# Performance work log

Hardware: AMD Instinct MI355X
Metric: run time of the kernel (lower is better)

## Reference

```python
import jax, jax.numpy as jnp
import numpy as np

D = 768
H = 12
DH = D // H  # 64
LN_EPS = 1e-5


def layer_norm(x, gamma, beta):
    mu = jnp.mean(x, axis=-1, keepdims=True)
    var = jnp.var(x, axis=-1, keepdims=True)
    return (x - mu) * jax.lax.rsqrt(var + LN_EPS) * gamma + beta


def setup_inputs() -> dict:
    key = jax.random.key(0)
    ks = jax.random.split(key, 12)
    b, n1, n2 = 2, 4096, 4096
    s = 1.0 / np.sqrt(D)
    return {
        "input_cap": jax.random.normal(ks[0], (b, n1, D), jnp.float32),
        "output_cap": jax.random.normal(ks[1], (b, n2, D), jnp.float32),
        "Wq": jax.random.normal(ks[2], (D, D), jnp.float32) * s,
        "bq": jnp.zeros((D,), jnp.float32),
        "Wk": jax.random.normal(ks[3], (D, D), jnp.float32) * s,
        "bk": jnp.zeros((D,), jnp.float32),
        "Wv": jax.random.normal(ks[4], (D, D), jnp.float32) * s,
        "bv": jnp.zeros((D,), jnp.float32),
        "ln_g": jnp.ones((D,), jnp.float32),
        "ln_b": jnp.zeros((D,), jnp.float32),
        "Wp": jax.random.normal(ks[5], (D, D), jnp.float32) * s,
        "bp": jnp.zeros((D,), jnp.float32),
    }


def reference(input_cap, output_cap, Wq, bq, Wk, bk, Wv, bv, ln_g, ln_b, Wp, bp):
    b, n1, _ = input_cap.shape
    n2 = output_cap.shape[1]
    i = layer_norm(input_cap, ln_g, ln_b)   # shared LayerNorm, as in source
    o = layer_norm(output_cap, ln_g, ln_b)
    q = (o @ Wq.T + bq).reshape(b, n2, H, DH).transpose(0, 2, 1, 3)  # b h n2 dh
    k = (i @ Wk.T + bk).reshape(b, n1, H, DH).transpose(0, 2, 1, 3)  # b h n1 dh
    v = (i @ Wv.T + bv).reshape(b, n1, H, DH).transpose(0, 2, 1, 3)  # b h n1 dh
    scores = jnp.einsum("bhqd,bhkd->bhqk", q, k) / np.sqrt(DH)
    probs = jax.nn.softmax(scores, axis=-1)
    ctl = jnp.einsum("bhqk,bhkd->bhqd", probs, v)
    ctl = ctl.transpose(0, 2, 1, 3).reshape(b, n2, D)
    # DropPath is identity in eval mode
    return output_cap + ctl @ Wp.T + bp
```

## Files before the change

kernel.cpp:

```cpp
#include <hip/hip_runtime.h>


#define D 768
#define LDP 72
#define L2E 1.4426950408889634f
#define NW 589824

typedef unsigned int u32;
typedef unsigned short u16;
typedef short bf16x8 __attribute__((ext_vector_type(8)));
typedef float f32x4 __attribute__((ext_vector_type(4)));
typedef float f32x16 __attribute__((ext_vector_type(16)));
typedef u16 u16x4 __attribute__((ext_vector_type(4)));
typedef u32 u32x4 __attribute__((ext_vector_type(4)));
typedef float f32x4v __attribute__((ext_vector_type(4)));

static __device__ __forceinline__ u16 f2bf(float f) {
  u32 b = __builtin_bit_cast(u32, f);
  b += 0x7FFFu + ((b >> 16) & 1u);
  return (u16)(b >> 16);
}

static __device__ __forceinline__ u32 cvtpk(float lo, float hi) {
  u32 r;
  asm("v_cvt_pk_bf16_f32 %0, %1, %2" : "=v"(r) : "v"(lo), "v"(hi));
  return r;
}

static __device__ __forceinline__ void plswap(u32& a, u32& b) {
  asm("v_permlane32_swap_b32 %0, %1" : "+v"(a), "+v"(b));
}

#define MFMA16(a, b, c) __builtin_amdgcn_mfma_f32_16x16x32_bf16((a), (b), (c), 0, 0, 0)
#define MFMA32(a, b, c) __builtin_amdgcn_mfma_f32_32x32x16_bf16((a), (b), (c), 0, 0, 0)

__global__ __launch_bounds__(256) void ln_kernel(
    const float* __restrict__ icap, const float* __restrict__ ocap,
    const float* __restrict__ g, const float* __restrict__ be,
    u16* __restrict__ iln, u16* __restrict__ oln) {
  int r = blockIdx.x;
  const float* src; u16* dst; int rr;
  if (r < 8192) { src = icap; dst = iln; rr = r; }
  else          { src = ocap; dst = oln; rr = r - 8192; }
  const float* row = src + (size_t)rr * D;
  int t = threadIdx.x;
  float x0 = row[t], x1 = row[t + 256], x2 = row[t + 512];
  float s = x0 + x1 + x2;
  float q = x0 * x0 + x1 * x1 + x2 * x2;
#pragma unroll
  for (int off = 32; off > 0; off >>= 1) {
    s += __shfl_xor(s, off);
    q += __shfl_xor(q, off);
  }
  __shared__ float red[8];
  int w = t >> 6, lane = t & 63;
  if (lane == 0) { red[w] = s; red[4 + w] = q; }
  __syncthreads();
  s = red[0] + red[1] + red[2] + red[3];
  q = red[4] + red[5] + red[6] + red[7];
  float mu = s * (1.0f / 768.0f);
  float var = q * (1.0f / 768.0f) - mu * mu;
  float rs = rsqrtf(var + 1e-5f);
  u16* drow = dst + (size_t)rr * D;
  drow[t]       = f2bf((x0 - mu) * rs * g[t]       + be[t]);
  drow[t + 256] = f2bf((x1 - mu) * rs * g[t + 256] + be[t + 256]);
  drow[t + 512] = f2bf((x2 - mu) * rs * g[t + 512] + be[t + 512]);
}

__global__ __launch_bounds__(256) void wcast_kernel(
    const float* __restrict__ w0, const float* __restrict__ w1,
    const float* __restrict__ w2, const float* __restrict__ w3,
    u16* __restrict__ dst) {
  int wsel = blockIdx.y;
  const float* src = wsel == 0 ? w0 : wsel == 1 ? w1 : wsel == 2 ? w2 : w3;
  int i = (blockIdx.x * 256 + threadIdx.x) * 4;
  f32x4v v = *(const f32x4v*)(src + i);
  u16x4 o = { f2bf(v[0]), f2bf(v[1]), f2bf(v[2]), f2bf(v[3]) };
  *(u16x4*)(dst + (size_t)wsel * NW + i) = o;
}

static __device__ __forceinline__ void gemm_core_128(
    const u16* __restrict__ A, const u16* __restrict__ W,
    int mrow0, int nrow0, f32x4 (&acc)[4][4]) {
  __shared__ __align__(16) u16 As[128][LDP];
  __shared__ __align__(16) u16 Bs[128][LDP];
  const int tid = threadIdx.x;
  const int lane = tid & 63;
  const int w = tid >> 6;
  const int wr = (w >> 1) << 6, wc = (w & 1) << 6;
  const int l15 = lane & 15, lg = lane >> 4;

  for (int kt = 0; kt < D; kt += 64) {
#pragma unroll
    for (int it = 0; it < 4; ++it) {
      int idx = it * 256 + tid;
      int row = idx >> 3, c8 = (idx & 7) << 3;
      uint4 va = *(const uint4*)(A + (size_t)(mrow0 + row) * D + kt + c8);
      uint4 vb = *(const uint4*)(W + (size_t)(nrow0 + row) * D + kt + c8);
      *(uint4*)&As[row][c8] = va;
      *(uint4*)&Bs[row][c8] = vb;
    }
    __syncthreads();
    bf16x8 af[4][2];
#pragma unroll
    for (int m = 0; m < 4; ++m) {
#pragma unroll
      for (int c = 0; c < 2; ++c)
        af[m][c] = *(const bf16x8*)&As[wr + m * 16 + l15][c * 32 + lg * 8];
    }
#pragma unroll
    for (int n = 0; n < 4; ++n) {
      bf16x8 b0 = *(const bf16x8*)&Bs[wc + n * 16 + l15][lg * 8];
      bf16x8 b1 = *(const bf16x8*)&Bs[wc + n * 16 + l15][32 + lg * 8];
#pragma unroll
      for (int m = 0; m < 4; ++m) {
        acc[m][n] = MFMA16(af[m][0], b0, acc[m][n]);
        acc[m][n] = MFMA16(af[m][1], b1, acc[m][n]);
      }
    }
    __syncthreads();
  }
}

__global__ __launch_bounds__(256) void qkv_gemm(
    const u16* __restrict__ i_ln, const u16* __restrict__ o_ln,
    const u16* __restrict__ Wb,
    const float* __restrict__ bq, const float* __restrict__ bk,
    const float* __restrict__ bv,
    u16* __restrict__ qout, u16* __restrict__ kout, u16* __restrict__ vT) {
  const int mblk = blockIdx.x;
  const int ny = blockIdx.y;
  const int which = ny / 6;
  const int nb = ny % 6;
  const u16* A = (which == 0) ? o_ln : i_ln;
  const u16* W = Wb + (size_t)which * NW;
  const float* bias = (which == 0) ? bq : (which == 1) ? bk : bv;

  const f32x4 z = {0.f, 0.f, 0.f, 0.f};
  f32x4 acc[4][4];
#pragma unroll
  for (int m = 0; m < 4; ++m)
#pragma unroll
    for (int n = 0; n < 4; ++n) acc[m][n] = z;

  gemm_core_128(A, W, mblk * 128, nb * 128, acc);

  const int lane = threadIdx.x & 63, w = threadIdx.x >> 6;
  const int wr = (w >> 1) << 6, wc = (w & 1) << 6;
  const int l15 = lane & 15, lg = lane >> 4;
  const int m0 = mblk * 128 + wr;
  const int n0 = nb * 128 + wc;

  if (which == 2) {
#pragma unroll
    for (int m = 0; m < 4; ++m) {
#pragma unroll
      for (int n = 0; n < 4; ++n) {
        int gn = n0 + n * 16 + l15;
        float bi = bias[gn];
        int gm = m0 + m * 16 + lg * 4;
        int bidx = gm >> 12, seq = gm & 4095;
        u16x4 pk = { f2bf(acc[m][n][0] + bi), f2bf(acc[m][n][1] + bi),
                     f2bf(acc[m][n][2] + bi), f2bf(acc[m][n][3] + bi) };
        *(u16x4*)(vT + ((size_t)bidx * 768 + gn) * 4096 + seq) = pk;
      }
    }
  } else {
    u16* out = (which == 0) ? qout : kout;
    const float scale = (which == 0) ? 0.125f : 1.0f;
#pragma unroll
    for (int m = 0; m < 4; ++m) {
#pragma unroll
      for (int n = 0; n < 4; ++n) {
        int gn = n0 + n * 16 + l15;
        float bi = bias[gn];
#pragma unroll
        for (int r = 0; r < 4; ++r) {
          int gm = m0 + m * 16 + lg * 4 + r;
          out[(size_t)gm * D + gn] = f2bf((acc[m][n][r] + bi) * scale);
        }
      }
    }
  }
}

__global__ __launch_bounds__(256) void proj_gemm(
    const u16* __restrict__ ctl, const u16* __restrict__ Wpb,
    const float* __restrict__ bp, const float* __restrict__ res,
    float* __restrict__ out) {
  const int mblk = blockIdx.x;
  const int nb = blockIdx.y;
  const f32x4 z = {0.f, 0.f, 0.f, 0.f};
  f32x4 acc[4][4];
#pragma unroll
  for (int m = 0; m < 4; ++m)
#pragma unroll
    for (int n = 0; n < 4; ++n) acc[m][n] = z;

  gemm_core_128(ctl, Wpb, mblk * 128, nb * 128, acc);

  const int lane = threadIdx.x & 63, w = threadIdx.x >> 6;
  const int wr = (w >> 1) << 6, wc = (w & 1) << 6;
  const int l15 = lane & 15, lg = lane >> 4;
  const int m0 = mblk * 128 + wr;
  const int n0 = nb * 128 + wc;
#pragma unroll
  for (int m = 0; m < 4; ++m) {
#pragma unroll
    for (int n = 0; n < 4; ++n) {
      int gn = n0 + n * 16 + l15;
      float bi = bp[gn];
#pragma unroll
      for (int r = 0; r < 4; ++r) {
        int gm = m0 + m * 16 + lg * 4 + r;
        out[(size_t)gm * D + gn] = res[(size_t)gm * D + gn] + acc[m][n][r] + bi;
      }
    }
  }
}

__global__ __launch_bounds__(256, 3) void attn_kernel(
    const u16* __restrict__ q, const u16* __restrict__ k,
    const u16* __restrict__ vT, u16* __restrict__ ctl) {
  const int qb = blockIdx.x;
  const int bh = blockIdx.y;
  const int b = bh / 12, h = bh % 12;
  const int tid = threadIdx.x;
  const int lane = tid & 63, w = tid >> 6;
  const int l31 = lane & 31;
  const int hi = lane >> 5;
  const int swz = l31 & 7;

  __shared__ __align__(16) u16 Ks[64 * 64];
  __shared__ __align__(16) u16 Vs[64 * 64];

  const int qrow0 = qb * 128 + w * 32;
  const u16* qbase = q + (size_t)b * 4096 * D + h * 64;
  const u16* kbase = k + (size_t)b * 4096 * D + h * 64;
  const u16* vbase = vT + ((size_t)b * 768 + h * 64) * 4096;

  bf16x8 qf[4];
#pragma unroll
  for (int ks = 0; ks < 4; ++ks)
    qf[ks] = *(const bf16x8*)(qbase + (size_t)(qrow0 + l31) * D + ks * 16 + hi * 8);

  f32x16 acc[2];
#pragma unroll
  for (int db = 0; db < 2; ++db)
#pragma unroll
    for (int r = 0; r < 16; ++r) acc[db][r] = 0.f;
  float m = -1e30f, l = 0.f;

  for (int kv0 = 0; kv0 < 4096; kv0 += 64) {
#pragma unroll
    for (int it = 0; it < 2; ++it) {
      int idx = it * 256 + tid;
      int row = idx >> 3, c16 = idx & 7;
      int sc = c16 ^ (row & 7);
      uint4 vk = *(const uint4*)(kbase + (size_t)(kv0 + row) * D + c16 * 8);
      uint4 vv = *(const uint4*)(vbase + (size_t)row * 4096 + kv0 + c16 * 8);
      *(uint4*)&Ks[row * 64 + sc * 8] = vk;
      *(uint4*)&Vs[row * 64 + sc * 8] = vv;
    }
    __syncthreads();

    f32x16 st[2];
#pragma unroll
    for (int t = 0; t < 2; ++t) {
      f32x16 s;
#pragma unroll
      for (int r = 0; r < 16; ++r) s[r] = 0.f;
#pragma unroll
      for (int ks = 0; ks < 4; ++ks) {
        bf16x8 kf = *(const bf16x8*)&Ks[(t * 32 + l31) * 64 + ((2 * ks + hi) ^ swz) * 8];
        s = MFMA32(kf, qf[ks], s);
      }
      st[t] = s;
    }

    float pm = st[0][0];
#pragma unroll
    for (int t = 0; t < 2; ++t)
#pragma unroll
      for (int r = 0; r < 16; ++r) pm = fmaxf(pm, st[t][r]);
    { u32 a = __builtin_bit_cast(u32, pm), bb = a;
      plswap(a, bb);
      float po = __builtin_bit_cast(float, hi ? a : bb);
      pm = fmaxf(pm, po); }

    if (pm > m + 8.0f) {
      float es = __builtin_amdgcn_exp2f((m - pm) * L2E);
      m = pm;
      l *= es;
#pragma unroll
      for (int db = 0; db < 2; ++db)
#pragma unroll
        for (int r = 0; r < 16; ++r) acc[db][r] *= es;
    }
    float mL2 = m * L2E;

    float ls = 0.f;
    bf16x8 pf[4];
#pragma unroll
    for (int t = 0; t < 2; ++t) {
      float p[16];
#pragma unroll
      for (int r = 0; r < 16; ++r) {
        p[r] = __builtin_amdgcn_exp2f(st[t][r] * L2E - mL2);
        ls += p[r];
      }
      u32 a0 = cvtpk(p[0], p[1]),   a1 = cvtpk(p[2], p[3]);
      u32 b0 = cvtpk(p[4], p[5]),   b1 = cvtpk(p[6], p[7]);
      plswap(a0, b0); plswap(a1, b1);
      u32x4 w0 = {a0, a1, b0, b1};
      pf[2 * t] = __builtin_bit_cast(bf16x8, w0);
      u32 c0 = cvtpk(p[8], p[9]),   c1 = cvtpk(p[10], p[11]);
      u32 d0 = cvtpk(p[12], p[13]), d1 = cvtpk(p[14], p[15]);
      plswap(c0, d0); plswap(c1, d1);
      u32x4 w1 = {c0, c1, d0, d1};
      pf[2 * t + 1] = __builtin_bit_cast(bf16x8, w1);
    }
    { u32 a = __builtin_bit_cast(u32, ls), bb = a;
      plswap(a, bb);
      float lo = __builtin_bit_cast(float, hi ? a : bb);
      ls += lo; }
    l += ls;

#pragma unroll
    for (int db = 0; db < 2; ++db)
#pragma unroll
      for (int ks = 0; ks < 4; ++ks) {
        bf16x8 vf = *(const bf16x8*)&Vs[(db * 32 + l31) * 64 + ((2 * ks + hi) ^ swz) * 8];
        acc[db] = MFMA32(vf, pf[ks], acc[db]);
      }
    __syncthreads();
  }

  float inv = 1.0f / l;
  u16* cbase = ctl + ((size_t)b * 4096 + qrow0 + l31) * D + h * 64;
#pragma unroll
  for (int db = 0; db < 2; ++db)
#pragma unroll
    for (int rq = 0; rq < 4; ++rq) {
      u16x4 pkv = { f2bf(acc[db][rq * 4 + 0] * inv), f2bf(acc[db][rq * 4 + 1] * inv),
                    f2bf(acc[db][rq * 4 + 2] * inv), f2bf(acc[db][rq * 4 + 3] * inv) };
      *(u16x4*)(cbase + db * 32 + rq * 8 + hi * 4) = pkv;
    }
}

extern "C" void kernel_launch(void* const* d_in, const int* in_sizes, int n_in,
                              void* d_out, int out_size, void* d_ws, size_t ws_size,
                              hipStream_t stream) {
  const float* in_cap  = (const float*)d_in[0];
  const float* out_cap = (const float*)d_in[1];
  const float* Wq = (const float*)d_in[2];
  const float* bq = (const float*)d_in[3];
  const float* Wk = (const float*)d_in[4];
  const float* bk = (const float*)d_in[5];
  const float* Wv = (const float*)d_in[6];
  const float* bv = (const float*)d_in[7];
  const float* ln_g = (const float*)d_in[8];
  const float* ln_b = (const float*)d_in[9];
  const float* Wp = (const float*)d_in[10];
  const float* bp = (const float*)d_in[11];
  float* out = (float*)d_out;

  char* ws = (char*)d_ws;
  const size_t tsz = (size_t)8192 * D * 2;
  u16* i_ln = (u16*)(ws + 0 * tsz);
  u16* o_ln = (u16*)(ws + 1 * tsz);
  u16* qb_  = (u16*)(ws + 2 * tsz);
  u16* kb_  = (u16*)(ws + 3 * tsz);
  u16* vT   = (u16*)(ws + 4 * tsz);
  u16* ctl  = (u16*)(ws + 5 * tsz);
  u16* Wb   = (u16*)(ws + 6 * tsz);

  ln_kernel<<<dim3(16384), dim3(256), 0, stream>>>(in_cap, out_cap, ln_g, ln_b, i_ln, o_ln);
  wcast_kernel<<<dim3(576, 4), dim3(256), 0, stream>>>(Wq, Wk, Wv, Wp, Wb);
  qkv_gemm<<<dim3(64, 18), dim3(256), 0, stream>>>(i_ln, o_ln, Wb, bq, bk, bv, qb_, kb_, vT);
  attn_kernel<<<dim3(32, 24), dim3(256), 0, stream>>>(qb_, kb_, vT, ctl);
  proj_gemm<<<dim3(64, 6), dim3(256), 0, stream>>>(ctl, Wb + (size_t)3 * NW, bp, out_cap, out);
}
```

Baseline: 344.0 us.

## Use direct global-to-LDS loads in GEMM and prefetch K/V tiles in attention

In the projection GEMM core, the register-staged tile copy is replaced with global_load_lds 16-byte direct loads into unpadded 64-wide LDS tiles. The attention loop now prefetches the next K/V tile into registers while the current tile is computed, which overlaps global load latency with MFMA work. The loop also wraps the MFMA sections in s_setprio and splits the max and sum reductions into four independent chains to shorten dependency chains. Dropping the LDS row padding may add bank conflicts on fragment reads, and the prefetch raises register pressure.

```diff
diff --git a/kernel.cpp b/kernel.cpp
--- a/kernel.cpp
+++ b/kernel.cpp
@@ -2,7 +2,6 @@
 
 
 #define D 768
-#define LDP 72
 #define L2E 1.4426950408889634f
 #define NW 589824
 
@@ -29,6 +28,12 @@
 
 static __device__ __forceinline__ void plswap(u32& a, u32& b) {
   asm("v_permlane32_swap_b32 %0, %1" : "+v"(a), "+v"(b));
+}
+
+static __device__ __forceinline__ void gload_lds16(const u16* g, u16* l) {
+  __builtin_amdgcn_global_load_lds(
+      (const __attribute__((address_space(1))) unsigned int*)g,
+      (__attribute__((address_space(3))) unsigned int*)l, 16, 0, 0);
 }
 
 #define MFMA16(a, b, c) __builtin_amdgcn_mfma_f32_16x16x32_bf16((a), (b), (c), 0, 0, 0)
@@ -82,23 +87,23 @@
 static __device__ __forceinline__ void gemm_core_128(
     const u16* __restrict__ A, const u16* __restrict__ W,
     int mrow0, int nrow0, f32x4 (&acc)[4][4]) {
-  __shared__ __align__(16) u16 As[128][LDP];
-  __shared__ __align__(16) u16 Bs[128][LDP];
+  __shared__ __align__(1024) u16 As[128 * 64];
+  __shared__ __align__(1024) u16 Bs[128 * 64];
   const int tid = threadIdx.x;
   const int lane = tid & 63;
   const int w = tid >> 6;
   const int wr = (w >> 1) << 6, wc = (w & 1) << 6;
   const int l15 = lane & 15, lg = lane >> 4;
+  const int lr = lane >> 3, lc = (lane & 7) << 3;
 
   for (int kt = 0; kt < D; kt += 64) {
 #pragma unroll
-    for (int it = 0; it < 4; ++it) {
-      int idx = it * 256 + tid;
-      int row = idx >> 3, c8 = (idx & 7) << 3;
-      uint4 va = *(const uint4*)(A + (size_t)(mrow0 + row) * D + kt + c8);
-      uint4 vb = *(const uint4*)(W + (size_t)(nrow0 + row) * D + kt + c8);
-      *(uint4*)&As[row][c8] = va;
-      *(uint4*)&Bs[row][c8] = vb;
+    for (int j = 0; j < 4; ++j) {
+      int c = w * 4 + j;
+      const u16* ga = A + (size_t)(mrow0 + c * 8 + lr) * D + kt + lc;
+      const u16* gb = W + (size_t)(nrow0 + c * 8 + lr) * D + kt + lc;
+      gload_lds16(ga, &As[c * 512]);
+      gload_lds16(gb, &Bs[c * 512]);
     }
     __syncthreads();
     bf16x8 af[4][2];
@@ -106,12 +111,12 @@
     for (int m = 0; m < 4; ++m) {
 #pragma unroll
       for (int c = 0; c < 2; ++c)
-        af[m][c] = *(const bf16x8*)&As[wr + m * 16 + l15][c * 32 + lg * 8];
+        af[m][c] = *(const bf16x8*)&As[(wr + m * 16 + l15) * 64 + c * 32 + lg * 8];
     }
 #pragma unroll
     for (int n = 0; n < 4; ++n) {
-      bf16x8 b0 = *(const bf16x8*)&Bs[wc + n * 16 + l15][lg * 8];
-      bf16x8 b1 = *(const bf16x8*)&Bs[wc + n * 16 + l15][32 + lg * 8];
+      bf16x8 b0 = *(const bf16x8*)&Bs[(wc + n * 16 + l15) * 64 + lg * 8];
+      bf16x8 b1 = *(const bf16x8*)&Bs[(wc + n * 16 + l15) * 64 + 32 + lg * 8];
 #pragma unroll
       for (int m = 0; m < 4; ++m) {
         acc[m][n] = MFMA16(af[m][0], b0, acc[m][n]);
@@ -251,20 +256,31 @@
     for (int r = 0; r < 16; ++r) acc[db][r] = 0.f;
   float m = -1e30f, l = 0.f;
 
+  const int r0 = tid >> 3, c0 = tid & 7;
+  const int sc8 = (c0 ^ (r0 & 7)) << 3;
+  uint4 vk0, vk1, vv0, vv1;
+  vk0 = *(const uint4*)(kbase + (size_t)r0 * D + c0 * 8);
+  vv0 = *(const uint4*)(vbase + (size_t)r0 * 4096 + c0 * 8);
+  vk1 = *(const uint4*)(kbase + (size_t)(r0 + 32) * D + c0 * 8);
+  vv1 = *(const uint4*)(vbase + (size_t)(r0 + 32) * 4096 + c0 * 8);
+
   for (int kv0 = 0; kv0 < 4096; kv0 += 64) {
-#pragma unroll
-    for (int it = 0; it < 2; ++it) {
-      int idx = it * 256 + tid;
-      int row = idx >> 3, c16 = idx & 7;
-      int sc = c16 ^ (row & 7);
-      uint4 vk = *(const uint4*)(kbase + (size_t)(kv0 + row) * D + c16 * 8);
-      uint4 vv = *(const uint4*)(vbase + (size_t)row * 4096 + kv0 + c16 * 8);
-      *(uint4*)&Ks[row * 64 + sc * 8] = vk;
-      *(uint4*)&Vs[row * 64 + sc * 8] = vv;
-    }
+    *(uint4*)&Ks[r0 * 64 + sc8] = vk0;
+    *(uint4*)&Vs[r0 * 64 + sc8] = vv0;
+    *(uint4*)&Ks[(r0 + 32) * 64 + sc8] = vk1;
+    *(uint4*)&Vs[(r0 + 32) * 64 + sc8] = vv1;
     __syncthreads();
 
+    if (kv0 + 64 < 4096) {
+      int nx = kv0 + 64;
+      vk0 = *(const uint4*)(kbase + (size_t)(nx + r0) * D + c0 * 8);
+      vv0 = *(const uint4*)(vbase + (size_t)r0 * 4096 + nx + c0 * 8);
+      vk1 = *(const uint4*)(kbase + (size_t)(nx + r0 + 32) * D + c0 * 8);
+      vv1 = *(const uint4*)(vbase + (size_t)(r0 + 32) * 4096 + nx + c0 * 8);
+    }
+
     f32x16 st[2];
+    __builtin_amdgcn_s_setprio(1);
 #pragma unroll
     for (int t = 0; t < 2; ++t) {
       f32x16 s;
@@ -277,12 +293,20 @@
       }
       st[t] = s;
     }
-
-    float pm = st[0][0];
-#pragma unroll
-    for (int t = 0; t < 2; ++t)
-#pragma unroll
-      for (int r = 0; r < 16; ++r) pm = fmaxf(pm, st[t][r]);
+    __builtin_amdgcn_s_setprio(0);
+
+    float pmA = st[0][0], pmB = st[0][1], pmC = st[0][2], pmD = st[0][3];
+#pragma unroll
+    for (int r = 4; r < 16; r += 4) {
+      pmA = fmaxf(pmA, st[0][r]);     pmB = fmaxf(pmB, st[0][r + 1]);
+      pmC = fmaxf(pmC, st[0][r + 2]); pmD = fmaxf(pmD, st[0][r + 3]);
+    }
+#pragma unroll
+    for (int r = 0; r < 16; r += 4) {
+      pmA = fmaxf(pmA, st[1][r]);     pmB = fmaxf(pmB, st[1][r + 1]);
+      pmC = fmaxf(pmC, st[1][r + 2]); pmD = fmaxf(pmD, st[1][r + 3]);
+    }
+    float pm = fmaxf(fmaxf(pmA, pmB), fmaxf(pmC, pmD));
     { u32 a = __builtin_bit_cast(u32, pm), bb = a;
       plswap(a, bb);
       float po = __builtin_bit_cast(float, hi ? a : bb);
@@ -299,33 +323,38 @@
     }
     float mL2 = m * L2E;
 
-    float ls = 0.f;
+    float ls0 = 0.f, ls1 = 0.f, ls2 = 0.f, ls3 = 0.f;
     bf16x8 pf[4];
 #pragma unroll
     for (int t = 0; t < 2; ++t) {
       float p[16];
 #pragma unroll
-      for (int r = 0; r < 16; ++r) {
-        p[r] = __builtin_amdgcn_exp2f(st[t][r] * L2E - mL2);
-        ls += p[r];
+      for (int r = 0; r < 16; r += 4) {
+        p[r]     = __builtin_amdgcn_exp2f(st[t][r] * L2E - mL2);
+        p[r + 1] = __builtin_amdgcn_exp2f(st[t][r + 1] * L2E - mL2);
+        p[r + 2] = __builtin_amdgcn_exp2f(st[t][r + 2] * L2E - mL2);
+        p[r + 3] = __builtin_amdgcn_exp2f(st[t][r + 3] * L2E - mL2);
+        ls0 += p[r]; ls1 += p[r + 1]; ls2 += p[r + 2]; ls3 += p[r + 3];
       }
       u32 a0 = cvtpk(p[0], p[1]),   a1 = cvtpk(p[2], p[3]);
       u32 b0 = cvtpk(p[4], p[5]),   b1 = cvtpk(p[6], p[7]);
       plswap(a0, b0); plswap(a1, b1);
       u32x4 w0 = {a0, a1, b0, b1};
       pf[2 * t] = __builtin_bit_cast(bf16x8, w0);
-      u32 c0 = cvtpk(p[8], p[9]),   c1 = cvtpk(p[10], p[11]);
+      u32 c0_ = cvtpk(p[8], p[9]),   c1 = cvtpk(p[10], p[11]);
       u32 d0 = cvtpk(p[12], p[13]), d1 = cvtpk(p[14], p[15]);
-      plswap(c0, d0); plswap(c1, d1);
-      u32x4 w1 = {c0, c1, d0, d1};
+      plswap(c0_, d0); plswap(c1, d1);
+      u32x4 w1 = {c0_, c1, d0, d1};
       pf[2 * t + 1] = __builtin_bit_cast(bf16x8, w1);
     }
+    float ls = (ls0 + ls1) + (ls2 + ls3);
     { u32 a = __builtin_bit_cast(u32, ls), bb = a;
       plswap(a, bb);
       float lo = __builtin_bit_cast(float, hi ? a : bb);
       ls += lo; }
     l += ls;
 
+    __builtin_amdgcn_s_setprio(1);
 #pragma unroll
     for (int db = 0; db < 2; ++db)
 #pragma unroll
@@ -333,6 +362,7 @@
         bf16x8 vf = *(const bf16x8*)&Vs[(db * 32 + l31) * 64 + ((2 * ks + hi) ^ swz) * 8];
         acc[db] = MFMA32(vf, pf[ks], acc[db]);
       }
+    __builtin_amdgcn_s_setprio(0);
     __syncthreads();
   }
 
```

Result: no change. 350.3 us (+1.8%).
